# Kernel tuning notes

Hardware: AMD Instinct MI355X
Metric: run time of the kernel (lower is better)

## Reference

```python
import jax, jax.numpy as jnp
import numpy as np

DIM = 768
NUM_HEADS = 12
HEAD_DIM = DIM // NUM_HEADS
SCALE = HEAD_DIM ** -0.5
NEG = -9e15


def setup_inputs() -> dict:
    key = jax.random.key(0)
    ks = jax.random.split(key, 8)
    B, N, M, C = 4, 1024, 2048, DIM
    q = jax.random.normal(ks[0], (B, N, C), dtype=jnp.float32)
    kv = jax.random.normal(ks[1], (B, M, C), dtype=jnp.float32)
    mask = jax.random.randint(ks[2], (B, 1, N, M), 0, 2, dtype=jnp.int32)
    s = 1.0 / np.sqrt(C)
    Wq = jax.random.normal(ks[3], (C, C), dtype=jnp.float32) * s      # nn.Linear(dim, dim), no bias
    Wkv = jax.random.normal(ks[4], (2 * C, C), dtype=jnp.float32) * s  # nn.Linear(dim, 2*dim), no bias
    Wproj = jax.random.normal(ks[5], (C, C), dtype=jnp.float32) * s
    bproj = jax.random.normal(ks[6], (C,), dtype=jnp.float32) * s
    return {"q": q, "kv": kv, "Wq": Wq, "Wkv": Wkv, "Wproj": Wproj, "bproj": bproj, "mask": mask}


def reference(q, kv, Wq, Wkv, Wproj, bproj, mask):
    B, M, C = kv.shape
    _, N, _ = q.shape
    H, d = NUM_HEADS, HEAD_DIM
    # kv projection -> [B, M, 2, H, d] -> k, v: [B, H, M, d]
    kvp = (kv @ Wkv.T).reshape(B, M, 2, H, d)
    k = kvp[:, :, 0].transpose(0, 2, 1, 3)
    v = kvp[:, :, 1].transpose(0, 2, 1, 3)
    # q projection -> [B, H, N, d], pre-scaled
    qp = (q @ Wq.T).reshape(B, N, H, d).transpose(0, 2, 1, 3) * SCALE
    attn = jnp.einsum('bhnd,bhmd->bhnm', qp, k)  # [B, H, N, M]
    attn = jnp.where(mask == 0, NEG, attn)
    attn = jax.nn.softmax(attn, axis=-1)
    # attn_drop / proj_drop have rate 0.0 (eval): identity
    x = jnp.einsum('bhnm,bhmd->bhnd', attn, v)
    x = x.transpose(0, 2, 1, 3).reshape(B, N, C)
    x = x @ Wproj.T + bproj
    return x
```

## Files before the change

### kernel.cpp

```cpp
#include <hip/hip_runtime.h>
#include <hip/hip_bf16.h>


typedef short    s16x8  __attribute__((ext_vector_type(8)));
typedef short    s16x4  __attribute__((ext_vector_type(4)));
typedef float    f32x4  __attribute__((ext_vector_type(4)));
typedef _Float16 f16x8  __attribute__((ext_vector_type(8)));
typedef _Float16 f16x4  __attribute__((ext_vector_type(4)));
typedef _Float16 f16x2  __attribute__((ext_vector_type(2)));

#define NUM_H 12
#define DIM   768
#define NQ    1024
#define MK    2048
#define QK_SCALE_LOG2E 0.18033688f

__device__ __forceinline__ short f2h(float v) {
    _Float16 h = (_Float16)v;
    return __builtin_bit_cast(short, h);
}
__device__ __forceinline__ f32x4 mfma16x32(f16x8 a, f16x8 b, f32x4 c) {
    return __builtin_amdgcn_mfma_f32_16x16x32_f16(a, b, c, 0, 0, 0);
}
__device__ __forceinline__ f16x2 pk2h(float a, float b) {
    return __builtin_bit_cast(f16x2, __builtin_amdgcn_cvt_pkrtz(a, b));
}

__global__ __launch_bounds__(256) void prep_kernel(
    const float* __restrict__ q, const float* __restrict__ kv,
    const float* __restrict__ Wq, const float* __restrict__ Wkv,
    const float* __restrict__ Wp, const int* __restrict__ mask,
    short* __restrict__ q_h, short* __restrict__ kv_h,
    short* __restrict__ Wq_h, short* __restrict__ Wkv_h,
    short* __restrict__ Wp_h, unsigned char* __restrict__ mbytes)
{
    int bid = blockIdx.x;
    if (bid < 5760) {
        const float* s; short* d; long base;
        if (bid < 1536)      { s = q;   d = q_h;   base = (long)bid * 2048; }
        else if (bid < 4608) { s = kv;  d = kv_h;  base = (long)(bid - 1536) * 2048; }
        else if (bid < 4896) { s = Wq;  d = Wq_h;  base = (long)(bid - 4608) * 2048; }
        else if (bid < 5472) { s = Wkv; d = Wkv_h; base = (long)(bid - 4896) * 2048; }
        else                 { s = Wp;  d = Wp_h;  base = (long)(bid - 5472) * 2048; }
        long i = base + threadIdx.x * 8;
        float4 a = *(const float4*)(s + i);
        float4 b = *(const float4*)(s + i + 4);
        s16x8 r;
        r[0] = f2h(a.x); r[1] = f2h(a.y); r[2] = f2h(a.z); r[3] = f2h(a.w);
        r[4] = f2h(b.x); r[5] = f2h(b.y); r[6] = f2h(b.z); r[7] = f2h(b.w);
        *(s16x8*)(d + i) = r;
    } else {
        long base = (long)(bid - 5760) * 2048 + threadIdx.x * 8;
        int4 m0 = *(const int4*)(mask + base);
        int4 m1 = *(const int4*)(mask + base + 4);
        unsigned v = (unsigned)(m0.x != 0)        | ((unsigned)(m0.y != 0) << 1)
                   | ((unsigned)(m0.z != 0) << 2) | ((unsigned)(m0.w != 0) << 3)
                   | ((unsigned)(m1.x != 0) << 4) | ((unsigned)(m1.y != 0) << 5)
                   | ((unsigned)(m1.z != 0) << 6) | ((unsigned)(m1.w != 0) << 7);
        mbytes[base >> 3] = (unsigned char)v;
    }
}

__device__ __forceinline__ void gemm_core(
    short* smem,
    const short* __restrict__ A, const short* __restrict__ Bt,
    int Ncols, int mode, const float* __restrict__ bias,
    short* __restrict__ outb, short* __restrict__ outb2,
    float* __restrict__ outf, int bid)
{
    short (*As)[72] = (short(*)[72])smem;
    short (*Bs)[72] = (short(*)[72])(smem + 9216);

    int ntiles = Ncols >> 7;
    int m0 = (bid / ntiles) << 7;
    int n0 = (bid % ntiles) << 7;
    int t = threadIdx.x;
    int w = t >> 6, lane = t & 63, quad = lane >> 4, l16 = lane & 15;
    int wm = (w & 1) << 6, wn = (w >> 1) << 6;

    f32x4 zero4 = {0.f, 0.f, 0.f, 0.f};
    f32x4 acc[4][4];
    for (int i = 0; i < 4; i++)
        for (int j = 0; j < 4; j++) acc[i][j] = zero4;

    int lr = t >> 1;
    int lc = (t & 1) << 5;
    const short* Ap = A + (long)(m0 + lr) * DIM + lc;
    const short* Bp = Bt + (long)(n0 + lr) * DIM + lc;

    s16x8 a0[4], b0[4], a1[4], b1[4];
    #pragma unroll
    for (int c = 0; c < 4; c++) {
        a0[c] = *(const s16x8*)(Ap + c * 8);
        b0[c] = *(const s16x8*)(Bp + c * 8);
        a1[c] = *(const s16x8*)(Ap + 64 + c * 8);
        b1[c] = *(const s16x8*)(Bp + 64 + c * 8);
    }

    auto mfma_tile = [&]() {
        #pragma unroll
        for (int kh = 0; kh < 2; kh++) {
            f16x8 af[4], bfr[4];
            #pragma unroll
            for (int i = 0; i < 4; i++)
                af[i] = __builtin_bit_cast(f16x8,
                    *(const s16x8*)&As[wm + i * 16 + l16][kh * 32 + quad * 8]);
            #pragma unroll
            for (int j = 0; j < 4; j++)
                bfr[j] = __builtin_bit_cast(f16x8,
                    *(const s16x8*)&Bs[wn + j * 16 + l16][kh * 32 + quad * 8]);
            #pragma unroll
            for (int i = 0; i < 4; i++)
                #pragma unroll
                for (int j = 0; j < 4; j++)
                    acc[i][j] = mfma16x32(af[i], bfr[j], acc[i][j]);
        }
    };

    for (int kt = 0; kt < DIM; kt += 128) {
        __syncthreads();
        #pragma unroll
        for (int c = 0; c < 4; c++) {
            *(s16x8*)&As[lr][lc + c * 8] = a0[c];
            *(s16x8*)&Bs[lr][lc + c * 8] = b0[c];
        }
        __syncthreads();
        if (kt + 128 < DIM) {
            #pragma unroll
            for (int c = 0; c < 4; c++) {
                a0[c] = *(const s16x8*)(Ap + kt + 128 + c * 8);
                b0[c] = *(const s16x8*)(Bp + kt + 128 + c * 8);
            }
        }
        mfma_tile();
        __syncthreads();
        #pragma unroll
        for (int c = 0; c < 4; c++) {
            *(s16x8*)&As[lr][lc + c * 8] = a1[c];
            *(s16x8*)&Bs[lr][lc + c * 8] = b1[c];
        }
        __syncthreads();
        if (kt + 192 < DIM) {
            #pragma unroll
            for (int c = 0; c < 4; c++) {
                a1[c] = *(const s16x8*)(Ap + kt + 192 + c * 8);
                b1[c] = *(const s16x8*)(Bp + kt + 192 + c * 8);
            }
        }
        mfma_tile();
    }

    __syncthreads();

    if (mode == 2) {
        #pragma unroll
        for (int i = 0; i < 4; i++)
            #pragma unroll
            for (int j = 0; j < 4; j++)
                #pragma unroll
                for (int r = 0; r < 4; r++) {
                    int row = m0 + wm + i * 16 + quad * 4 + r;
                    int col = n0 + wn + j * 16 + l16;
                    outf[(long)row * DIM + col] = acc[i][j][r] + bias[col];
                }
        return;
    }

    short (*Cs)[136] = (short(*)[136])smem;
    bool vreg = (mode == 1) && (n0 >= DIM);

    if (!vreg) {
        float sc = (mode == 0) ? QK_SCALE_LOG2E : 1.0f;
        #pragma unroll
        for (int i = 0; i < 4; i++)
            #pragma unroll
            for (int j = 0; j < 4; j++)
                #pragma unroll
                for (int r = 0; r < 4; r++)
                    Cs[wm + i * 16 + quad * 4 + r][wn + j * 16 + l16] =
                        f2h(acc[i][j][r] * sc);
    } else {
        #pragma unroll
        for (int i = 0; i < 4; i++)
            #pragma unroll
            for (int j = 0; j < 4; j++) {
                int c = wn + j * 16 + l16;
                int r0 = wm + i * 16 + quad * 4;
                s16x4 pk;
                pk[0] = f2h(acc[i][j][0]); pk[1] = f2h(acc[i][j][1]);
                pk[2] = f2h(acc[i][j][2]); pk[3] = f2h(acc[i][j][3]);
                *(s16x4*)&Cs[c][r0] = pk;
            }
    }
    __syncthreads();

    if (!vreg) {
        int hb2 = n0 >> 6;
        long rowsN = (mode == 0) ? NQ : MK;
        int b = (int)(m0 / rowsN);
        int rb = (int)(m0 % rowsN);
        short* ob0 = outb + ((long)(b * NUM_H + hb2) * rowsN + rb) * 64;
        short* ob1 = outb + ((long)(b * NUM_H + hb2 + 1) * rowsN + rb) * 64;
        #pragma unroll
        for (int k2 = 0; k2 < 8; k2++) {
            int ch = k2 * 256 + t;
            int half = ch >> 10, off = ch & 1023;
            s16x8 vd = *(const s16x8*)&Cs[off >> 3][(half << 6) + ((off & 7) << 3)];
            *(s16x8*)((half ? ob1 : ob0) + off * 8) = vd;
        }
    } else {
        int hb2 = (n0 - DIM) >> 6;
        int b = m0 >> 11, rb = m0 & 2047;
        #pragma unroll
        for (int k2 = 0; k2 < 8; k2++) {
            int ch = k2 * 256 + t;
            int c = ch >> 4, woff = (ch & 15) << 3;
            s16x8 vd = *(const s16x8*)&Cs[c][woff];
            int half = c >> 6, dd = c & 63;
            *(s16x8*)(outb2 + (((long)(b * NUM_H + hb2 + half) * 64 + dd) * MK + rb) + woff) = vd;
        }
    }
}

__global__ __launch_bounds__(256) void gemm12_kernel(
    const short* __restrict__ qh, const short* __restrict__ Wqh,
    const short* __restrict__ kvh, const short* __restrict__ Wkvh,
    short* __restrict__ qp, short* __restrict__ kk, short* __restrict__ vt)
{
    __shared__ short smem[18432];
    if (blockIdx.x < 192)
        gemm_core(smem, qh, Wqh, 768, 0, nullptr, qp, nullptr, nullptr, blockIdx.x);
    else
        gemm_core(smem, kvh, Wkvh, 1536, 1, nullptr, kk, vt, nullptr, blockIdx.x - 192);
}

__global__ __launch_bounds__(256) void gemm3_kernel(
    const short* __restrict__ xb, const short* __restrict__ Wph,
    const float* __restrict__ bias, float* __restrict__ out)
{
    __shared__ short smem[18432];
    gemm_core(smem, xb, Wph, 768, 2, bias, nullptr, nullptr, out, blockIdx.x);
}

__global__ __launch_bounds__(256) void attn_kernel(
    const short* __restrict__ qp, const short* __restrict__ kk,
    const short* __restrict__ vt, const unsigned* __restrict__ mb,
    short* __restrict__ xb)
{
    __shared__ short qs[64][72];
    __shared__ short ks[64][64];
    __shared__ short vs[64][64];

    int bid = blockIdx.x;
    int bh = bid % 48;
    int nt = bid / 48;
    int h = bh % NUM_H, b = bh / NUM_H;
    int n0 = nt << 6;
    int t = threadIdx.x, w = t >> 6, lane = t & 63, quad = lane >> 4, l16 = lane & 15;

    const short* qbase = qp + ((long)bh * NQ + n0) * 64;
    const short* kbase = kk + (long)bh * MK * 64;
    const short* vbase = vt + (long)bh * 64 * MK;
    const unsigned* mrow = mb + ((long)b * NQ + n0 + (w << 4) + l16) * 64;

    {
        int qr = t >> 2, c0 = (t & 3) << 4;
        *(s16x8*)&qs[qr][c0]     = *(const s16x8*)(qbase + qr * 64 + c0);
        *(s16x8*)&qs[qr][c0 + 8] = *(const s16x8*)(qbase + qr * 64 + c0 + 8);
    }
    __syncthreads();
    f16x8 bq[2];
    #pragma unroll
    for (int kh = 0; kh < 2; kh++)
        bq[kh] = __builtin_bit_cast(f16x8,
            *(const s16x8*)&qs[(w << 4) + l16][kh * 32 + quad * 8]);

    int sr = t >> 2, c0 = (t & 3) << 4;
    int pr = (sr & 32) + ((sr & 4) << 2) + ((sr & 24) >> 1) + (sr & 3);
    int swk = (pr & 7) << 3;
    int swv = (sr & 7) << 3;
    int swl = (l16 & 7) << 3;
    const short* kp = kbase + (long)sr * 64 + c0;
    const short* vp = vbase + (long)sr * MK + c0;

    s16x8 k0 = *(const s16x8*)(kp);
    s16x8 k1 = *(const s16x8*)(kp + 8);
    s16x8 v0 = *(const s16x8*)(vp);
    s16x8 v1 = *(const s16x8*)(vp + 8);
    uint2 mwv = *(const uint2*)(mrow);

    f32x4 zero4 = {0.f, 0.f, 0.f, 0.f};
    f32x4 o[4], ol = zero4;
    for (int j = 0; j < 4; j++) o[j] = zero4;
    const f16x8 ones = {(_Float16)1.f, (_Float16)1.f, (_Float16)1.f, (_Float16)1.f,
                        (_Float16)1.f, (_Float16)1.f, (_Float16)1.f, (_Float16)1.f};

    for (int mt = 0; mt < MK; mt += 64) {
        __syncthreads();
        *(s16x8*)&ks[pr][c0 ^ swk]       = k0;
        *(s16x8*)&ks[pr][(c0 + 8) ^ swk] = k1;
        *(s16x8*)&vs[sr][c0 ^ swv]       = v0;
        *(s16x8*)&vs[sr][(c0 + 8) ^ swv] = v1;
        unsigned cm0 = mwv.x, cm1 = mwv.y;
        __syncthreads();
        if (mt + 64 < MK) {
            k0 = *(const s16x8*)(kp + (long)(mt + 64) * 64);
            k1 = *(const s16x8*)(kp + (long)(mt + 64) * 64 + 8);
            v0 = *(const s16x8*)(vp + mt + 64);
            v1 = *(const s16x8*)(vp + mt + 64 + 8);
            mwv = *(const uint2*)(mrow + ((mt + 64) >> 5));
        }

        f32x4 s[4];
        #pragma unroll
        for (int jj = 0; jj < 4; jj++) s[jj] = zero4;
        __builtin_amdgcn_s_setprio(1);
        #pragma unroll
        for (int kh = 0; kh < 2; kh++)
            #pragma unroll
            for (int jj = 0; jj < 4; jj++) {
                f16x8 ak = __builtin_bit_cast(f16x8,
                    *(const s16x8*)&ks[jj * 16 + l16][(kh * 32 + quad * 8) ^ swl]);
                s[jj] = mfma16x32(ak, bq[kh], s[jj]);
            }
        __builtin_amdgcn_s_setprio(0);

        f16x8 pa[2];
        #pragma unroll
        for (int j2 = 0; j2 < 2; j2++) {
            unsigned wsel = j2 ? cm1 : cm0;
            f16x2 pk[4];
            #pragma unroll
            for (int sub = 0; sub < 2; sub++) {
                unsigned bits = wsel >> ((quad << 3) + (sub << 2));
                const f32x4& sv = s[j2 * 2 + sub];
                float p0 = (bits & 1u)        ? __builtin_amdgcn_exp2f(sv[0]) : 0.f;
                float p1 = ((bits >> 1) & 1u) ? __builtin_amdgcn_exp2f(sv[1]) : 0.f;
                float p2 = ((bits >> 2) & 1u) ? __builtin_amdgcn_exp2f(sv[2]) : 0.f;
                float p3 = ((bits >> 3) & 1u) ? __builtin_amdgcn_exp2f(sv[3]) : 0.f;
                pk[sub * 2]     = pk2h(p0, p1);
                pk[sub * 2 + 1] = pk2h(p2, p3);
            }
            f16x4 lo = __builtin_shufflevector(pk[0], pk[1], 0, 1, 2, 3);
            f16x4 hi = __builtin_shufflevector(pk[2], pk[3], 0, 1, 2, 3);
            pa[j2] = __builtin_shufflevector(lo, hi, 0, 1, 2, 3, 4, 5, 6, 7);
        }

        __builtin_amdgcn_s_setprio(1);
        #pragma unroll
        for (int j2 = 0; j2 < 2; j2++) {
            ol = mfma16x32(pa[j2], ones, ol);
            #pragma unroll
            for (int jd = 0; jd < 4; jd++) {
                f16x8 bv = __builtin_bit_cast(f16x8,
                    *(const s16x8*)&vs[jd * 16 + l16][(j2 * 32 + quad * 8) ^ swl]);
                o[jd] = mfma16x32(pa[j2], bv, o[jd]);
            }
        }
        __builtin_amdgcn_s_setprio(0);
    }

    float linv[4];
    #pragma unroll
    for (int rr = 0; rr < 4; rr++) linv[rr] = 1.0f / ol[rr];
    short (*ps)[72] = (short(*)[72])&qs[w << 4];
    #pragma unroll
    for (int jd = 0; jd < 4; jd++)
        #pragma unroll
        for (int rr = 0; rr < 4; rr++)
            ps[quad * 4 + rr][jd * 16 + l16] = f2h(o[jd][rr] * linv[rr]);

    #pragma unroll
    for (int k2 = 0; k2 < 2; k2++) {
        int row = (lane >> 3) + k2 * 8;
        int cc = (lane & 7) << 3;
        s16x8 vd = *(const s16x8*)&ps[row][cc];
        *(s16x8*)(xb + ((long)b * NQ + n0 + (w << 4) + row) * DIM + h * 64 + cc) = vd;
    }
}

extern "C" void kernel_launch(void* const* d_in, const int* in_sizes, int n_in,
                              void* d_out, int out_size, void* d_ws, size_t ws_size,
                              hipStream_t stream)
{
    const float* q     = (const float*)d_in[0];
    const float* kv    = (const float*)d_in[1];
    const float* Wq    = (const float*)d_in[2];
    const float* Wkv   = (const float*)d_in[3];
    const float* Wproj = (const float*)d_in[4];
    const float* bproj = (const float*)d_in[5];
    const int*   mask  = (const int*)d_in[6];
    float* out = (float*)d_out;

    char* ws = (char*)d_ws;
    short* q_h   = (short*)ws; ws += (size_t)4096 * 768 * 2;
    short* kv_h  = (short*)ws; ws += (size_t)8192 * 768 * 2;
    short* Wq_h  = (short*)ws; ws += (size_t)768 * 768 * 2;
    short* Wkv_h = (short*)ws; ws += (size_t)1536 * 768 * 2;
    short* Wp_h  = (short*)ws; ws += (size_t)768 * 768 * 2;
    short* qp    = (short*)ws; ws += (size_t)4096 * 768 * 2;
    short* kk    = (short*)ws; ws += (size_t)8192 * 768 * 2;
    short* vt    = (short*)ws; ws += (size_t)8192 * 768 * 2;
    short* xb    = (short*)ws; ws += (size_t)4096 * 768 * 2;
    unsigned char* mbytes = (unsigned char*)ws;

    prep_kernel<<<9856, 256, 0, stream>>>(q, kv, Wq, Wkv, Wproj, mask,
                                          q_h, kv_h, Wq_h, Wkv_h, Wp_h, mbytes);
    gemm12_kernel<<<960, 256, 0, stream>>>(q_h, Wq_h, kv_h, Wkv_h, qp, kk, vt);
    attn_kernel<<<768, 256, 0, stream>>>(qp, kk, vt, (const unsigned*)mbytes, xb);
    gemm3_kernel<<<192, 256, 0, stream>>>(xb, Wp_h, bproj, out);
}
```

Before: 215.7 us.

## Split attention key range in two and add a partial-output reduction kernel

The attention kernel now splits the 2048-key range into two halves, doubling the grid from 768 to 1536 blocks. Each block writes its unnormalized fp32 partial output and its row sums to scratch. A new reduce kernel adds the two halves, normalizes, and writes the fp16 result. The aim is more blocks per CU for better latency hiding, paid for with extra global traffic for the partials and one more kernel launch. The partial buffer reuses workspace that already held the fp16 inputs, which are dead by this point.

```diff
diff --git a/kernel.cpp b/kernel.cpp
--- a/kernel.cpp
+++ b/kernel.cpp
@@ -245,7 +245,7 @@
 __global__ __launch_bounds__(256) void attn_kernel(
     const short* __restrict__ qp, const short* __restrict__ kk,
     const short* __restrict__ vt, const unsigned* __restrict__ mb,
-    short* __restrict__ xb)
+    float* __restrict__ po0, float* __restrict__ po1, float* __restrict__ pl)
 {
     __shared__ short qs[64][72];
     __shared__ short ks[64][64];
@@ -253,10 +253,14 @@
 
     int bid = blockIdx.x;
     int bh = bid % 48;
-    int nt = bid / 48;
+    int rest = bid / 48;
+    int nt = rest & 15;
+    int half = rest >> 4;
     int h = bh % NUM_H, b = bh / NUM_H;
     int n0 = nt << 6;
+    int mstart = half << 10;
     int t = threadIdx.x, w = t >> 6, lane = t & 63, quad = lane >> 4, l16 = lane & 15;
+    (void)h;
 
     const short* qbase = qp + ((long)bh * NQ + n0) * 64;
     const short* kbase = kk + (long)bh * MK * 64;
@@ -264,9 +268,9 @@
     const unsigned* mrow = mb + ((long)b * NQ + n0 + (w << 4) + l16) * 64;
 
     {
-        int qr = t >> 2, c0 = (t & 3) << 4;
-        *(s16x8*)&qs[qr][c0]     = *(const s16x8*)(qbase + qr * 64 + c0);
-        *(s16x8*)&qs[qr][c0 + 8] = *(const s16x8*)(qbase + qr * 64 + c0 + 8);
+        int qr = t >> 2, c0q = (t & 3) << 4;
+        *(s16x8*)&qs[qr][c0q]     = *(const s16x8*)(qbase + qr * 64 + c0q);
+        *(s16x8*)&qs[qr][c0q + 8] = *(const s16x8*)(qbase + qr * 64 + c0q + 8);
     }
     __syncthreads();
     f16x8 bq[2];
@@ -280,14 +284,14 @@
     int swk = (pr & 7) << 3;
     int swv = (sr & 7) << 3;
     int swl = (l16 & 7) << 3;
-    const short* kp = kbase + (long)sr * 64 + c0;
-    const short* vp = vbase + (long)sr * MK + c0;
+    const short* kp = kbase + (long)(mstart + sr) * 64 + c0;
+    const short* vp = vbase + (long)sr * MK + mstart + c0;
 
     s16x8 k0 = *(const s16x8*)(kp);
     s16x8 k1 = *(const s16x8*)(kp + 8);
     s16x8 v0 = *(const s16x8*)(vp);
     s16x8 v1 = *(const s16x8*)(vp + 8);
-    uint2 mwv = *(const uint2*)(mrow);
+    uint2 mwv = *(const uint2*)(mrow + (mstart >> 5));
 
     f32x4 zero4 = {0.f, 0.f, 0.f, 0.f};
     f32x4 o[4], ol = zero4;
@@ -295,7 +299,7 @@
     const f16x8 ones = {(_Float16)1.f, (_Float16)1.f, (_Float16)1.f, (_Float16)1.f,
                         (_Float16)1.f, (_Float16)1.f, (_Float16)1.f, (_Float16)1.f};
 
-    for (int mt = 0; mt < MK; mt += 64) {
+    for (int mt = 0; mt < 1024; mt += 64) {
         __syncthreads();
         *(s16x8*)&ks[pr][c0 ^ swk]       = k0;
         *(s16x8*)&ks[pr][(c0 + 8) ^ swk] = k1;
@@ -303,12 +307,12 @@
         *(s16x8*)&vs[sr][(c0 + 8) ^ swv] = v1;
         unsigned cm0 = mwv.x, cm1 = mwv.y;
         __syncthreads();
-        if (mt + 64 < MK) {
+        if (mt + 64 < 1024) {
             k0 = *(const s16x8*)(kp + (long)(mt + 64) * 64);
             k1 = *(const s16x8*)(kp + (long)(mt + 64) * 64 + 8);
             v0 = *(const s16x8*)(vp + mt + 64);
             v1 = *(const s16x8*)(vp + mt + 64 + 8);
-            mwv = *(const uint2*)(mrow + ((mt + 64) >> 5));
+            mwv = *(const uint2*)(mrow + ((mstart + mt + 64) >> 5));
         }
 
         f32x4 s[4];
@@ -360,23 +364,47 @@
         __builtin_amdgcn_s_setprio(0);
     }
 
-    float linv[4];
-    #pragma unroll
-    for (int rr = 0; rr < 4; rr++) linv[rr] = 1.0f / ol[rr];
-    short (*ps)[72] = (short(*)[72])&qs[w << 4];
+    float* poh = (half ? po1 : po0)
+               + ((long)bh * NQ + n0 + (w << 4)) * 64;
     #pragma unroll
     for (int jd = 0; jd < 4; jd++)
         #pragma unroll
         for (int rr = 0; rr < 4; rr++)
-            ps[quad * 4 + rr][jd * 16 + l16] = f2h(o[jd][rr] * linv[rr]);
-
-    #pragma unroll
-    for (int k2 = 0; k2 < 2; k2++) {
-        int row = (lane >> 3) + k2 * 8;
-        int cc = (lane & 7) << 3;
-        s16x8 vd = *(const s16x8*)&ps[row][cc];
-        *(s16x8*)(xb + ((long)b * NQ + n0 + (w << 4) + row) * DIM + h * 64 + cc) = vd;
-    }
+            poh[(quad * 4 + rr) * 64 + jd * 16 + l16] = o[jd][rr];
+    if (l16 == 0) {
+        float* plh = pl + (long)half * 48 * NQ + (long)bh * NQ + n0 + (w << 4);
+        #pragma unroll
+        for (int rr = 0; rr < 4; rr++)
+            plh[quad * 4 + rr] = ol[rr];
+    }
+}
+
+__global__ __launch_bounds__(256) void reduce_kernel(
+    const float* __restrict__ po0, const float* __restrict__ po1,
+    const float* __restrict__ pl, short* __restrict__ xb)
+{
+    int t = threadIdx.x;
+    int r = t >> 3;
+    int dp = (t & 7) << 3;
+    long grow = (long)blockIdx.x * 32 + r;
+    int bh = (int)(grow >> 10), n = (int)(grow & 1023);
+    const float* p0 = po0 + grow * 64 + dp;
+    const float* p1 = po1 + grow * 64 + dp;
+    float l = pl[grow] + pl[(long)48 * NQ + grow];
+    float inv = 1.0f / l;
+    float4 a0 = *(const float4*)p0, a1 = *(const float4*)(p0 + 4);
+    float4 b0 = *(const float4*)p1, b1 = *(const float4*)(p1 + 4);
+    s16x8 r8;
+    r8[0] = f2h((a0.x + b0.x) * inv);
+    r8[1] = f2h((a0.y + b0.y) * inv);
+    r8[2] = f2h((a0.z + b0.z) * inv);
+    r8[3] = f2h((a0.w + b0.w) * inv);
+    r8[4] = f2h((a1.x + b1.x) * inv);
+    r8[5] = f2h((a1.y + b1.y) * inv);
+    r8[6] = f2h((a1.z + b1.z) * inv);
+    r8[7] = f2h((a1.w + b1.w) * inv);
+    int b = bh / NUM_H, h = bh % NUM_H;
+    *(s16x8*)(xb + ((long)(b * NQ + n) * DIM + h * 64 + dp)) = r8;
 }
 
 extern "C" void kernel_launch(void* const* d_in, const int* in_sizes, int n_in,
@@ -402,11 +430,16 @@
     short* kk    = (short*)ws; ws += (size_t)8192 * 768 * 2;
     short* vt    = (short*)ws; ws += (size_t)8192 * 768 * 2;
     short* xb    = (short*)ws; ws += (size_t)4096 * 768 * 2;
-    unsigned char* mbytes = (unsigned char*)ws;
+    unsigned char* mbytes = (unsigned char*)ws; ws += (size_t)1 << 20;
+    float* po0 = (float*)d_ws;
+    float* po1 = (float*)ws; ws += (size_t)48 * 1024 * 64 * 4;
+    float* pl  = (float*)ws; ws += (size_t)2 * 48 * 1024 * 4;
 
     prep_kernel<<<9856, 256, 0, stream>>>(q, kv, Wq, Wkv, Wproj, mask,
                                           q_h, kv_h, Wq_h, Wkv_h, Wp_h, mbytes);
     gemm12_kernel<<<960, 256, 0, stream>>>(q_h, Wq_h, kv_h, Wkv_h, qp, kk, vt);
-    attn_kernel<<<768, 256, 0, stream>>>(qp, kk, vt, (const unsigned*)mbytes, xb);
+    attn_kernel<<<1536, 256, 0, stream>>>(qp, kk, vt, (const unsigned*)mbytes,
+                                          po0, po1, pl);
+    reduce_kernel<<<1536, 256, 0, stream>>>(po0, po1, pl, xb);
     gemm3_kernel<<<192, 256, 0, stream>>>(xb, Wp_h, bproj, out);
 }
```

New measurement: 220.1 us. 2.0% more time.

## Stage GEMM tiles via global_load_lds with XOR-swizzled LDS layout

Applied to the files above, without the earlier changes.

Replaces the register-staged double-buffered GEMM loads with direct global-to-LDS loads (global_load_lds, 16 bytes per lane) into an unpadded 64-wide tile whose 8-element chunks are XOR-swizzled to avoid bank conflicts. The K step drops from 128 (two halves held in registers) to 64, with the next tile issued after the compute barrier. This frees VGPRs and removes the register round-trip, but the load for the next tile is no longer overlapped with compute in a separate buffer, so latency may be more exposed.

```diff
diff --git a/kernel.cpp b/kernel.cpp
--- a/kernel.cpp
+++ b/kernel.cpp
@@ -68,8 +68,8 @@
     short* __restrict__ outb, short* __restrict__ outb2,
     float* __restrict__ outf, int bid)
 {
-    short (*As)[72] = (short(*)[72])smem;
-    short (*Bs)[72] = (short(*)[72])(smem + 9216);
+    short* As = smem;
+    short* Bs = smem + 8192;
 
     int ntiles = Ncols >> 7;
     int m0 = (bid / ntiles) << 7;
@@ -83,74 +83,52 @@
     for (int i = 0; i < 4; i++)
         for (int j = 0; j < 4; j++) acc[i][j] = zero4;
 
-    int lr = t >> 1;
-    int lc = (t & 1) << 5;
-    const short* Ap = A + (long)(m0 + lr) * DIM + lc;
-    const short* Bp = Bt + (long)(n0 + lr) * DIM + lc;
-
-    s16x8 a0[4], b0[4], a1[4], b1[4];
-    #pragma unroll
-    for (int c = 0; c < 4; c++) {
-        a0[c] = *(const s16x8*)(Ap + c * 8);
-        b0[c] = *(const s16x8*)(Bp + c * 8);
-        a1[c] = *(const s16x8*)(Ap + 64 + c * 8);
-        b1[c] = *(const s16x8*)(Bp + 64 + c * 8);
-    }
-
-    auto mfma_tile = [&]() {
+    int srow = (w << 3) + (lane >> 3);
+    int scol = (((lane & 7) ^ (lane >> 3)) << 3);
+    const short* Asrc = A + (long)(m0 + srow) * DIM + scol;
+    const short* Bsrc = Bt + (long)(n0 + srow) * DIM + scol;
+    short* Adst = As + (w << 9) + ((lane & 63) << 3);
+    short* Bdst = Bs + (w << 9) + ((lane & 63) << 3);
+
+    auto stage = [&](int kt) {
+        #pragma unroll
+        for (int i = 0; i < 4; i++) {
+            __builtin_amdgcn_global_load_lds(
+                (const unsigned int*)(Asrc + (long)i * 32 * DIM + kt),
+                (unsigned int*)(Adst + i * 2048), 16, 0, 0);
+            __builtin_amdgcn_global_load_lds(
+                (const unsigned int*)(Bsrc + (long)i * 32 * DIM + kt),
+                (unsigned int*)(Bdst + i * 2048), 16, 0, 0);
+        }
+    };
+
+    int swl = l16 & 7;
+
+    stage(0);
+    for (int kt = 0; kt < DIM; kt += 64) {
+        __syncthreads();
         #pragma unroll
         for (int kh = 0; kh < 2; kh++) {
             f16x8 af[4], bfr[4];
             #pragma unroll
             for (int i = 0; i < 4; i++)
-                af[i] = __builtin_bit_cast(f16x8,
-                    *(const s16x8*)&As[wm + i * 16 + l16][kh * 32 + quad * 8]);
+                af[i] = __builtin_bit_cast(f16x8, *(const s16x8*)(
+                    As + ((wm + i * 16 + l16) << 6)
+                       + ((((kh << 2) | quad) ^ swl) << 3)));
             #pragma unroll
             for (int j = 0; j < 4; j++)
-                bfr[j] = __builtin_bit_cast(f16x8,
-                    *(const s16x8*)&Bs[wn + j * 16 + l16][kh * 32 + quad * 8]);
+                bfr[j] = __builtin_bit_cast(f16x8, *(const s16x8*)(
+                    Bs + ((wn + j * 16 + l16) << 6)
+                       + ((((kh << 2) | quad) ^ swl) << 3)));
             #pragma unroll
             for (int i = 0; i < 4; i++)
                 #pragma unroll
                 for (int j = 0; j < 4; j++)
                     acc[i][j] = mfma16x32(af[i], bfr[j], acc[i][j]);
         }
-    };
-
-    for (int kt = 0; kt < DIM; kt += 128) {
         __syncthreads();
-        #pragma unroll
-        for (int c = 0; c < 4; c++) {
-            *(s16x8*)&As[lr][lc + c * 8] = a0[c];
-            *(s16x8*)&Bs[lr][lc + c * 8] = b0[c];
-        }
-        __syncthreads();
-        if (kt + 128 < DIM) {
-            #pragma unroll
-            for (int c = 0; c < 4; c++) {
-                a0[c] = *(const s16x8*)(Ap + kt + 128 + c * 8);
-                b0[c] = *(const s16x8*)(Bp + kt + 128 + c * 8);
-            }
-        }
-        mfma_tile();
-        __syncthreads();
-        #pragma unroll
-        for (int c = 0; c < 4; c++) {
-            *(s16x8*)&As[lr][lc + c * 8] = a1[c];
-            *(s16x8*)&Bs[lr][lc + c * 8] = b1[c];
-        }
-        __syncthreads();
-        if (kt + 192 < DIM) {
-            #pragma unroll
-            for (int c = 0; c < 4; c++) {
-                a1[c] = *(const s16x8*)(Ap + kt + 192 + c * 8);
-                b1[c] = *(const s16x8*)(Bp + kt + 192 + c * 8);
-            }
-        }
-        mfma_tile();
-    }
-
-    __syncthreads();
+        if (kt + 64 < DIM) stage(kt + 64);
+    }
 
     if (mode == 2) {
         #pragma unroll
@@ -264,9 +242,9 @@
     const unsigned* mrow = mb + ((long)b * NQ + n0 + (w << 4) + l16) * 64;
 
     {
-        int qr = t >> 2, c0 = (t & 3) << 4;
-        *(s16x8*)&qs[qr][c0]     = *(const s16x8*)(qbase + qr * 64 + c0);
-        *(s16x8*)&qs[qr][c0 + 8] = *(const s16x8*)(qbase + qr * 64 + c0 + 8);
+        int qr = t >> 2, c0q = (t & 3) << 4;
+        *(s16x8*)&qs[qr][c0q]     = *(const s16x8*)(qbase + qr * 64 + c0q);
+        *(s16x8*)&qs[qr][c0q + 8] = *(const s16x8*)(qbase + qr * 64 + c0q + 8);
     }
     __syncthreads();
     f16x8 bq[2];
```

Result: slower. 226.7 us (+5.1%).
